# Kernel optimization log

Measured on AMD Instinct MI355X. Metric: run time of the kernel, lower is better.

Reference implementation:

```python
import jax, jax.numpy as jnp
import numpy as np

BATCH = 2048
NUM_FIELDS = 32
EMBED = 64
NPAIRS = NUM_FIELDS * (NUM_FIELDS - 1) // 2  # 496
# static pair indices (i < j), same order as the torch double loop
ROW, COL = np.triu_indices(NUM_FIELDS, k=1)
ROW = jnp.asarray(ROW)
COL = jnp.asarray(COL)


def setup_inputs() -> dict:
    key = jax.random.key(0)
    k1, k2 = jax.random.split(key)
    emb_inputs = jax.random.normal(k1, (BATCH, NUM_FIELDS, EMBED), dtype=jnp.float32)
    # xavier_normal_ on kernel of shape (E, NC2, E): fan_in = NC2*E (dims[1:]), fan_out = E*E... 
    # torch: fan_in = size(1)*receptive = NPAIRS*EMBED? torch uses size(1)*prod(size[2:]) = NPAIRS*EMBED,
    # fan_out = size(0)*prod(size[2:]) = EMBED*EMBED; std = sqrt(2/(fan_in+fan_out))
    fan_in = NPAIRS * EMBED
    fan_out = EMBED * EMBED
    std = float(np.sqrt(2.0 / (fan_in + fan_out)))
    kernel = jax.random.normal(k2, (EMBED, NPAIRS, EMBED), dtype=jnp.float32) * std
    return {"emb_inputs": emb_inputs, "kernel": kernel}


def reference(emb_inputs, kernel):
    # emb_inputs: (B, N, E); kernel: (E, NC2, E)
    p = emb_inputs[:, ROW]  # (B, NC2, E)
    q = emb_inputs[:, COL]  # (B, NC2, E)
    # torch: kp[b,i,pair] = sum_j p[b,pair,j] * kernel[i,pair,j]; out[b,pair] = sum_i kp*q
    kp = jnp.einsum('bpj,ipj->bpi', p, kernel)  # (B, NC2, E) -- avoids (B,E,NC2,E) blowup
    outputs = jnp.sum(kp * q, axis=-1)          # (B, NC2)
    return outputs[:, None, :]                  # (B, 1, NC2)
```

## Files before the change

### kernel.cpp

```cpp
#include <hip/hip_runtime.h>
#include <hip/hip_bf16.h>

#define BATCH   2048
#define NFIELDS 32
#define EMBED   64
#define NPAIRS  496

typedef __attribute__((ext_vector_type(8))) short bf16x8;
typedef __attribute__((ext_vector_type(4))) float f32x4;

__device__ __forceinline__ unsigned short f2bf(float x) {
    unsigned int u = __float_as_uint(x);
    unsigned int r = 0x7fffu + ((u >> 16) & 1u);
    return (unsigned short)((u + r) >> 16);
}
__device__ __forceinline__ float bf2f(unsigned short b) {
    return __uint_as_float(((unsigned int)b) << 16);
}
__device__ __forceinline__ bf16x8 cvt8(const float* p) {
    float4 v0 = *(const float4*)p;
    float4 v1 = *(const float4*)(p + 4);
    bf16x8 o;
    o[0]=(short)f2bf(v0.x); o[1]=(short)f2bf(v0.y); o[2]=(short)f2bf(v0.z); o[3]=(short)f2bf(v0.w);
    o[4]=(short)f2bf(v1.x); o[5]=(short)f2bf(v1.y); o[6]=(short)f2bf(v1.z); o[7]=(short)f2bf(v1.w);
    return o;
}

__global__ __launch_bounds__(256) void convert_prepass(
    const float* __restrict__ emb, const float* __restrict__ kern,
    unsigned short* __restrict__ embB, unsigned short* __restrict__ kernB)
{
    const int EMB4 = BATCH * NFIELDS * EMBED / 4;
    const int KER4 = EMBED * NPAIRS * EMBED / 4;
    int t = blockIdx.x * blockDim.x + threadIdx.x;
    if (t < EMB4) {
        float4 v = ((const float4*)emb)[t];
        ushort4 o;
        o.x = f2bf(v.x); o.y = f2bf(v.y); o.z = f2bf(v.z); o.w = f2bf(v.w);
        *(ushort4*)(embB + (size_t)t * 4) = o;
    } else if (t < EMB4 + KER4) {
        int u = t - EMB4;
        int j4   = u & 15;
        int rest = u >> 4;
        int p = rest % NPAIRS;
        int i = rest / NPAIRS;
        float4 v = *(const float4*)(kern + (size_t)i * (NPAIRS*EMBED) + (size_t)p * EMBED + j4*4);
        ushort4 o;
        o.x = f2bf(v.x); o.y = f2bf(v.y); o.z = f2bf(v.z); o.w = f2bf(v.w);
        *(ushort4*)(kernB + (size_t)p * 4096 + i * 64 + j4 * 4) = o;
    }
}

template<bool PRE>
__global__ __launch_bounds__(256) void opn_main(
    const void* __restrict__ embP, const void* __restrict__ kernP,
    float* __restrict__ out)
{
    const int pair = blockIdx.x;
    const int bt   = blockIdx.y;

    int r = 0, s = 0;
    while (pair >= s + (NFIELDS - 1 - r)) { s += NFIELDS - 1 - r; ++r; }
    const int c = r + 1 + (pair - s);

    __shared__ __align__(16) unsigned short Klds[64][72];
    __shared__ __align__(16) unsigned short Alds[4][16][72];
    __shared__ __align__(16) unsigned short Qlds[4][16][72];

    const int tid = threadIdx.x;

    if (PRE) {
        const unsigned short* kb = (const unsigned short*)kernP + (size_t)pair * 4096;
        #pragma unroll
        for (int it = 0; it < 2; ++it) {
            int idx = (it * 256 + tid) * 8;
            int i = idx >> 6, j = idx & 63;
            *(bf16x8*)&Klds[i][j] = *(const bf16x8*)(kb + idx);
        }
    } else {
        const float* kf = (const float*)kernP;
        #pragma unroll
        for (int it = 0; it < 2; ++it) {
            int idx = (it * 256 + tid) * 8;
            int i = idx >> 6, j = idx & 63;
            const float* src = kf + (size_t)i * (NPAIRS*EMBED) + (size_t)pair * EMBED + j;
            *(bf16x8*)&Klds[i][j] = cvt8(src);
        }
    }
    __syncthreads();

    const int wave = tid >> 6, lane = tid & 63;
    const int col = lane & 15, quad = lane >> 4;

    bf16x8 bfr[4][2];
    #pragma unroll
    for (int nt = 0; nt < 4; ++nt)
        #pragma unroll
        for (int ks = 0; ks < 2; ++ks)
            bfr[nt][ks] = *(const bf16x8*)&Klds[nt*16 + col][ks*32 + quad*8];

    #pragma unroll
    for (int iter = 0; iter < 2; ++iter) {
        const int b0 = bt * 128 + iter * 64 + wave * 16;

        #pragma unroll
        for (int half = 0; half < 2; ++half) {
            int kk = half * 64 + lane;
            int row = kk >> 3, seg = kk & 7;
            size_t base = ((size_t)(b0 + row) * NFIELDS) * EMBED + (size_t)seg * 8;
            if (PRE) {
                const unsigned short* eb = (const unsigned short*)embP;
                *(bf16x8*)&Alds[wave][row][seg*8] = *(const bf16x8*)(eb + base + (size_t)r * EMBED);
                *(bf16x8*)&Qlds[wave][row][seg*8] = *(const bf16x8*)(eb + base + (size_t)c * EMBED);
            } else {
                const float* ef = (const float*)embP;
                *(bf16x8*)&Alds[wave][row][seg*8] = cvt8(ef + base + (size_t)r * EMBED);
                *(bf16x8*)&Qlds[wave][row][seg*8] = cvt8(ef + base + (size_t)c * EMBED);
            }
        }
        __syncthreads();

        bf16x8 afr0 = *(const bf16x8*)&Alds[wave][col][quad*8];
        bf16x8 afr1 = *(const bf16x8*)&Alds[wave][col][32 + quad*8];

        float partial[4] = {0.f, 0.f, 0.f, 0.f};
        #pragma unroll
        for (int nt = 0; nt < 4; ++nt) {
            f32x4 acc = {0.f, 0.f, 0.f, 0.f};
            acc = __builtin_amdgcn_mfma_f32_16x16x32_bf16(afr0, bfr[nt][0], acc, 0, 0, 0);
            acc = __builtin_amdgcn_mfma_f32_16x16x32_bf16(afr1, bfr[nt][1], acc, 0, 0, 0);
            #pragma unroll
            for (int rr = 0; rr < 4; ++rr) {
                float qv = bf2f(Qlds[wave][quad*4 + rr][nt*16 + col]);
                partial[rr] += acc[rr] * qv;
            }
        }
        #pragma unroll
        for (int mask = 1; mask <= 8; mask <<= 1)
            #pragma unroll
            for (int rr = 0; rr < 4; ++rr)
                partial[rr] += __shfl_xor(partial[rr], mask, 64);

        if (col == 0) {
            #pragma unroll
            for (int rr = 0; rr < 4; ++rr)
                out[(size_t)(b0 + quad*4 + rr) * NPAIRS + pair] = partial[rr];
        }
    }
}

extern "C" void kernel_launch(void* const* d_in, const int* in_sizes, int n_in,
                              void* d_out, int out_size, void* d_ws, size_t ws_size,
                              hipStream_t stream) {
    const float* emb  = (const float*)d_in[0];
    const float* kern = (const float*)d_in[1];
    float* out = (float*)d_out;

    const size_t embElems  = (size_t)BATCH * NFIELDS * EMBED;
    const size_t kernElems = (size_t)EMBED * NPAIRS * EMBED;
    const size_t need = (embElems + kernElems) * sizeof(unsigned short);

    dim3 grid(NPAIRS, BATCH / 128);
    if (ws_size >= need) {
        unsigned short* embB  = (unsigned short*)d_ws;
        unsigned short* kernB = embB + embElems;
        int total4 = (int)((embElems + kernElems) / 4);
        convert_prepass<<<(total4 + 255) / 256, 256, 0, stream>>>(emb, kern, embB, kernB);
        opn_main<true><<<grid, 256, 0, stream>>>((const void*)embB, (const void*)kernB, out);
    } else {
        opn_main<false><<<grid, 256, 0, stream>>>((const void*)emb, (const void*)kern, out);
    }
}
```

Baseline: 103.3 us.

## Swap MFMA operand roles, load embeddings directly to registers, drop LDS staging

The per-pair kernel is now the MFMA A operand and the embedding rows are the B operand. Each lane's output column maps to one batch element, so P and Q fragments are loaded straight from global memory into registers instead of being staged through shared memory. This removes the per-iteration syncthreads and LDS traffic, and the reduction needs two shuffles instead of sixteen. The batch tile per block also doubles to 256, which halves the grid and halves the number of times each kernel tile is loaded into LDS, at the cost of less coalesced direct global loads and fewer blocks.

```diff
diff --git a/kernel.cpp b/kernel.cpp
--- a/kernel.cpp
+++ b/kernel.cpp
@@ -5,6 +5,7 @@
 #define NFIELDS 32
 #define EMBED   64
 #define NPAIRS  496
+#define BT      256
 
 typedef __attribute__((ext_vector_type(8))) short bf16x8;
 typedef __attribute__((ext_vector_type(4))) float f32x4;
@@ -13,9 +14,6 @@
     unsigned int u = __float_as_uint(x);
     unsigned int r = 0x7fffu + ((u >> 16) & 1u);
     return (unsigned short)((u + r) >> 16);
-}
-__device__ __forceinline__ float bf2f(unsigned short b) {
-    return __uint_as_float(((unsigned int)b) << 16);
 }
 __device__ __forceinline__ bf16x8 cvt8(const float* p) {
     float4 v0 = *(const float4*)p;
@@ -59,32 +57,28 @@
     const int pair = blockIdx.x;
     const int bt   = blockIdx.y;
 
-    int r = 0, s = 0;
-    while (pair >= s + (NFIELDS - 1 - r)) { s += NFIELDS - 1 - r; ++r; }
-    const int c = r + 1 + (pair - s);
+    int r = 0, s0 = 0;
+    while (pair >= s0 + (NFIELDS - 1 - r)) { s0 += NFIELDS - 1 - r; ++r; }
+    const int c = r + 1 + (pair - s0);
 
     __shared__ __align__(16) unsigned short Klds[64][72];
-    __shared__ __align__(16) unsigned short Alds[4][16][72];
-    __shared__ __align__(16) unsigned short Qlds[4][16][72];
 
     const int tid = threadIdx.x;
 
     if (PRE) {
         const unsigned short* kb = (const unsigned short*)kernP + (size_t)pair * 4096;
         #pragma unroll
-        for (int it = 0; it < 2; ++it) {
-            int idx = (it * 256 + tid) * 8;
-            int i = idx >> 6, j = idx & 63;
-            *(bf16x8*)&Klds[i][j] = *(const bf16x8*)(kb + idx);
+        for (int itk = 0; itk < 2; ++itk) {
+            int idx = (itk * 256 + tid) * 8;
+            *(bf16x8*)&Klds[idx >> 6][idx & 63] = *(const bf16x8*)(kb + idx);
         }
     } else {
         const float* kf = (const float*)kernP;
         #pragma unroll
-        for (int it = 0; it < 2; ++it) {
-            int idx = (it * 256 + tid) * 8;
+        for (int itk = 0; itk < 2; ++itk) {
+            int idx = (itk * 256 + tid) * 8;
             int i = idx >> 6, j = idx & 63;
-            const float* src = kf + (size_t)i * (NPAIRS*EMBED) + (size_t)pair * EMBED + j;
-            *(bf16x8*)&Klds[i][j] = cvt8(src);
+            *(bf16x8*)&Klds[i][j] = cvt8(kf + (size_t)i * (NPAIRS*EMBED) + (size_t)pair * EMBED + j);
         }
     }
     __syncthreads();
@@ -92,60 +86,62 @@
     const int wave = tid >> 6, lane = tid & 63;
     const int col = lane & 15, quad = lane >> 4;
 
-    bf16x8 bfr[4][2];
+    bf16x8 kfr[4][2];
     #pragma unroll
-    for (int nt = 0; nt < 4; ++nt)
+    for (int mt = 0; mt < 4; ++mt)
         #pragma unroll
         for (int ks = 0; ks < 2; ++ks)
-            bfr[nt][ks] = *(const bf16x8*)&Klds[nt*16 + col][ks*32 + quad*8];
+            kfr[mt][ks] = *(const bf16x8*)&Klds[mt*16 + col][ks*32 + quad*8];
+
+    const unsigned short* eb = (const unsigned short*)embP;
+    const float* ef = (const float*)embP;
 
     #pragma unroll
-    for (int iter = 0; iter < 2; ++iter) {
-        const int b0 = bt * 128 + iter * 64 + wave * 16;
+    for (int it = 0; it < 4; ++it) {
+        const int b = bt * BT + wave * 64 + it * 16 + col;
+        const size_t rowbase = (size_t)b * (NFIELDS * EMBED);
 
+        bf16x8 pfr[2];
+        if (PRE) {
+            pfr[0] = *(const bf16x8*)(eb + rowbase + (size_t)r * EMBED + quad*8);
+            pfr[1] = *(const bf16x8*)(eb + rowbase + (size_t)r * EMBED + 32 + quad*8);
+        } else {
+            pfr[0] = cvt8(ef + rowbase + (size_t)r * EMBED + quad*8);
+            pfr[1] = cvt8(ef + rowbase + (size_t)r * EMBED + 32 + quad*8);
+        }
+
+        f32x4 acc[4];
         #pragma unroll
-        for (int half = 0; half < 2; ++half) {
-            int kk = half * 64 + lane;
-            int row = kk >> 3, seg = kk & 7;
-            size_t base = ((size_t)(b0 + row) * NFIELDS) * EMBED + (size_t)seg * 8;
+        for (int mt = 0; mt < 4; ++mt) {
+            acc[mt] = (f32x4){0.f, 0.f, 0.f, 0.f};
+            acc[mt] = __builtin_amdgcn_mfma_f32_16x16x32_bf16(kfr[mt][0], pfr[0], acc[mt], 0, 0, 0);
+            acc[mt] = __builtin_amdgcn_mfma_f32_16x16x32_bf16(kfr[mt][1], pfr[1], acc[mt], 0, 0, 0);
+        }
+
+        float partial = 0.f;
+        #pragma unroll
+        for (int mt = 0; mt < 4; ++mt) {
+            float qv0, qv1, qv2, qv3;
             if (PRE) {
-                const unsigned short* eb = (const unsigned short*)embP;
-                *(bf16x8*)&Alds[wave][row][seg*8] = *(const bf16x8*)(eb + base + (size_t)r * EMBED);
-                *(bf16x8*)&Qlds[wave][row][seg*8] = *(const bf16x8*)(eb + base + (size_t)c * EMBED);
+                uint2 qd = *(const uint2*)(eb + rowbase + (size_t)c * EMBED + mt*16 + quad*4);
+                qv0 = __uint_as_float(qd.x << 16);
+                qv1 = __uint_as_float(qd.x & 0xffff0000u);
+                qv2 = __uint_as_float(qd.y << 16);
+                qv3 = __uint_as_float(qd.y & 0xffff0000u);
             } else {
-                const float* ef = (const float*)embP;
-                *(bf16x8*)&Alds[wave][row][seg*8] = cvt8(ef + base + (size_t)r * EMBED);
-                *(bf16x8*)&Qlds[wave][row][seg*8] = cvt8(ef + base + (size_t)c * EMBED);
+                float4 qf = *(const float4*)(ef + rowbase + (size_t)c * EMBED + mt*16 + quad*4);
+                qv0 = qf.x; qv1 = qf.y; qv2 = qf.z; qv3 = qf.w;
             }
+            partial += acc[mt][0] * qv0;
+            partial += acc[mt][1] * qv1;
+            partial += acc[mt][2] * qv2;
+            partial += acc[mt][3] * qv3;
         }
-        __syncthreads();
+        partial += __shfl_xor(partial, 16, 64);
+        partial += __shfl_xor(partial, 32, 64);
 
-        bf16x8 afr0 = *(const bf16x8*)&Alds[wave][col][quad*8];
-        bf16x8 afr1 = *(const bf16x8*)&Alds[wave][col][32 + quad*8];
-
-        float partial[4] = {0.f, 0.f, 0.f, 0.f};
-        #pragma unroll
-        for (int nt = 0; nt < 4; ++nt) {
-            f32x4 acc = {0.f, 0.f, 0.f, 0.f};
-            acc = __builtin_amdgcn_mfma_f32_16x16x32_bf16(afr0, bfr[nt][0], acc, 0, 0, 0);
-            acc = __builtin_amdgcn_mfma_f32_16x16x32_bf16(afr1, bfr[nt][1], acc, 0, 0, 0);
-            #pragma unroll
-            for (int rr = 0; rr < 4; ++rr) {
-                float qv = bf2f(Qlds[wave][quad*4 + rr][nt*16 + col]);
-                partial[rr] += acc[rr] * qv;
-            }
-        }
-        #pragma unroll
-        for (int mask = 1; mask <= 8; mask <<= 1)
-            #pragma unroll
-            for (int rr = 0; rr < 4; ++rr)
-                partial[rr] += __shfl_xor(partial[rr], mask, 64);
-
-        if (col == 0) {
-            #pragma unroll
-            for (int rr = 0; rr < 4; ++rr)
-                out[(size_t)(b0 + quad*4 + rr) * NPAIRS + pair] = partial[rr];
-        }
+        if (quad == 0)
+            out[(size_t)b * NPAIRS + pair] = partial;
     }
 }
 
@@ -160,7 +156,7 @@
     const size_t kernElems = (size_t)EMBED * NPAIRS * EMBED;
     const size_t need = (embElems + kernElems) * sizeof(unsigned short);
 
-    dim3 grid(NPAIRS, BATCH / 128);
+    dim3 grid(NPAIRS, BATCH / BT);
     if (ws_size >= need) {
         unsigned short* embB  = (unsigned short*)d_ws;
         unsigned short* kernB = embB + embElems;
```

New measurement: 119.3 us. 1.16x slower.
